# Kernel optimization log

Hardware: AMD Instinct MI355X
Metric: run time of the kernel (lower is better)

The kernel has to match this reference:

```python
import jax, jax.numpy as jnp
import numpy as np

N_NODES = 100000
MAX_DEG = 16
D_IN = 256
D_OUT = 256


def setup_inputs() -> dict:
    key = jax.random.key(0)
    k1, k2, k3, k4, k5 = jax.random.split(key, 5)
    x = jax.random.normal(k1, (N_NODES, D_IN), dtype=jnp.float32)
    # padded edge list: -1 marks padding; first column always valid so degree >= 1
    col0 = jax.random.randint(k2, (N_NODES, 1), 0, N_NODES)
    rest = jax.random.randint(k3, (N_NODES, MAX_DEG - 1), -1, N_NODES)
    edge_index = jnp.concatenate([col0, rest], axis=1).astype(jnp.int64)
    # torch Linear(2*D_IN, D_OUT): weight [D_OUT, 2*D_IN], bias [D_OUT]
    W = jax.random.normal(k4, (D_OUT, 2 * D_IN), dtype=jnp.float32) * 0.05
    b = jax.random.normal(k5, (D_OUT,), dtype=jnp.float32) * 0.05
    return {"x": x, "edge_index": edge_index, "W": W, "b": b}


def reference(x, edge_index, W, b):
    # pad with a zero row so index -1 (padding) gathers zeros, matching torch
    padded = jnp.concatenate([x, jnp.zeros((1, x.shape[1]), dtype=x.dtype)], axis=0)
    neigh = padded[edge_index]  # [N, MAX_DEG, D_IN]
    degree = jnp.sum(edge_index >= 0, axis=-1, keepdims=True).astype(x.dtype)  # [N, 1]
    neigh_agg = jnp.sum(neigh, axis=1) / degree  # mean aggregation, [N, D_IN]
    h = jnp.concatenate([x, neigh_agg], axis=1)  # [N, 2*D_IN]
    return h @ W.T + b
```

## Files before the change

kernel.cpp:

```cpp
#include <hip/hip_runtime.h>
#include <stdint.h>


#define MAX_DEG 16
#define D_IN 256
#define D_K 512
#define D_OUT 256
#define BM 32
#define LDS_STRIDE 520
#define N_NODES_C 100000

typedef __attribute__((ext_vector_type(8))) short bf16x8;
typedef __attribute__((ext_vector_type(4))) float f32x4;

__device__ __forceinline__ uint32_t f2bf(float f) {
    union { float f; uint32_t u; } v; v.f = f;
    uint32_t u = v.u;
    return (u + 0x7FFFu + ((u >> 16) & 1u)) >> 16;
}
__device__ __forceinline__ uint32_t pack2(float lo, float hi) {
    return f2bf(lo) | (f2bf(hi) << 16);
}

__global__ __launch_bounds__(256) void cast_all_kernel(
    const float* __restrict__ x, const float* __restrict__ W,
    ushort* __restrict__ Xb, ushort* __restrict__ Wb)
{
    const int b = blockIdx.x;
    const int tid = threadIdx.x;
    if (b < 12500) {
        const size_t i = (size_t)b * 2048 + tid * 8;
        float4 v0 = *(const float4*)(x + i);
        float4 v1 = *(const float4*)(x + i + 4);
        uint4 p = { pack2(v0.x, v0.y), pack2(v0.z, v0.w),
                    pack2(v1.x, v1.y), pack2(v1.z, v1.w) };
        *(uint4*)(Xb + i) = p;
    } else if (b == 12500) {
        if (tid < 32) {
            uint4 z = {0u, 0u, 0u, 0u};
            *(uint4*)(Xb + (size_t)N_NODES_C * D_IN + tid * 8) = z;
        }
    } else {
        const size_t i = (size_t)(b - 12501) * 2048 + tid * 8;
        float4 v0 = *(const float4*)(W + i);
        float4 v1 = *(const float4*)(W + i + 4);
        uint4 p = { pack2(v0.x, v0.y), pack2(v0.z, v0.w),
                    pack2(v1.x, v1.y), pack2(v1.z, v1.w) };
        *(uint4*)(Wb + i) = p;
    }
}

__global__ __launch_bounds__(512, 4) void sage_bf16_kernel(
    const ushort* __restrict__ Xb,
    const int* __restrict__ edge,
    const ushort* __restrict__ Wb,
    const float* __restrict__ bias,
    float* __restrict__ out)
{
    __shared__ ushort sH[BM * LDS_STRIDE];

    const int tid = threadIdx.x;
    const int node0 = blockIdx.x * BM;

    {
        const int m = tid >> 4;
        const int l = tid & 15;
        const int node = node0 + m;

        const uint4* xr = (const uint4*)(Xb + (size_t)node * D_IN);
        uint4* selfdst = (uint4*)(sH + (size_t)m * LDS_STRIDE);
        uint4 s0 = xr[l], s1 = xr[16 + l];
        selfdst[l] = s0; selfdst[16 + l] = s1;

        const int4* ep = (const int4*)(edge + (size_t)node * MAX_DEG);
        uint32_t off[MAX_DEG]; int deg = 0;
        #pragma unroll
        for (int g = 0; g < 4; ++g) {
            int4 e = ep[g];
            deg += (e.x >= 0) + (e.y >= 0) + (e.z >= 0) + (e.w >= 0);
            off[g*4+0] = (uint32_t)(e.x < 0 ? N_NODES_C : e.x) * 512u;
            off[g*4+1] = (uint32_t)(e.y < 0 ? N_NODES_C : e.y) * 512u;
            off[g*4+2] = (uint32_t)(e.z < 0 ? N_NODES_C : e.z) * 512u;
            off[g*4+3] = (uint32_t)(e.w < 0 ? N_NODES_C : e.w) * 512u;
        }
        const float inv = 1.0f / (float)deg;
        const char* xb = (const char*)Xb;

        #pragma unroll 1
        for (int c = 0; c < 2; ++c) {
            const uint32_t coff = (uint32_t)(c * 256 + l * 16);
            uint4 st[MAX_DEG];
            #pragma unroll
            for (int d = 0; d < MAX_DEG; ++d)
                st[d] = *(const uint4*)(xb + (size_t)(off[d] + coff));

            float a[8];
            #pragma unroll
            for (int q = 0; q < 8; ++q) a[q] = 0.f;
            #pragma unroll
            for (int d = 0; d < MAX_DEG; ++d) {
                uint32_t u[4] = { st[d].x, st[d].y, st[d].z, st[d].w };
                #pragma unroll
                for (int q = 0; q < 4; ++q) {
                    union { uint32_t ui; float f; } lo, hi;
                    lo.ui = u[q] << 16;
                    hi.ui = u[q] & 0xFFFF0000u;
                    a[2*q]   += lo.f;
                    a[2*q+1] += hi.f;
                }
            }
            uint4 p = { pack2(a[0]*inv, a[1]*inv), pack2(a[2]*inv, a[3]*inv),
                        pack2(a[4]*inv, a[5]*inv), pack2(a[6]*inv, a[7]*inv) };
            *(uint4*)(sH + (size_t)m * LDS_STRIDE + D_IN + c * 128 + l * 8) = p;
        }
    }
    __syncthreads();

    {
        const int w = tid >> 6;
        const int lane = tid & 63;
        const int quad = lane >> 4;
        const int r16  = lane & 15;

        f32x4 acc[2][2];
        #pragma unroll
        for (int j = 0; j < 2; ++j) {
            float bv = bias[w * 32 + j * 16 + r16];
            acc[0][j] = (f32x4){bv, bv, bv, bv};
            acc[1][j] = (f32x4){bv, bv, bv, bv};
        }

        const ushort* a0p = sH + (size_t)r16 * LDS_STRIDE + quad * 8;
        const ushort* a1p = a0p + 16 * LDS_STRIDE;
        #pragma unroll
        for (int ks = 0; ks < D_K / 32; ++ks) {
            bf16x8 a0 = *(const bf16x8*)(a0p + ks * 32);
            bf16x8 a1 = *(const bf16x8*)(a1p + ks * 32);
            #pragma unroll
            for (int j = 0; j < 2; ++j) {
                const int o = w * 32 + j * 16 + r16;
                bf16x8 b = *(const bf16x8*)(Wb + (size_t)o * D_K + ks * 32 + quad * 8);
                acc[0][j] = __builtin_amdgcn_mfma_f32_16x16x32_bf16(a0, b, acc[0][j], 0, 0, 0);
                acc[1][j] = __builtin_amdgcn_mfma_f32_16x16x32_bf16(a1, b, acc[1][j], 0, 0, 0);
            }
        }

        #pragma unroll
        for (int mt = 0; mt < 2; ++mt) {
            #pragma unroll
            for (int j = 0; j < 2; ++j) {
                const int o = w * 32 + j * 16 + r16;
                #pragma unroll
                for (int r = 0; r < 4; ++r) {
                    const int row = node0 + mt * 16 + quad * 4 + r;
                    out[(size_t)row * D_OUT + o] = acc[mt][j][r];
                }
            }
        }
    }
}

__global__ __launch_bounds__(256) void cast_w_kernel(const float* __restrict__ W,
                                                     ushort* __restrict__ Wb) {
    int i = (blockIdx.x * 256 + threadIdx.x) * 4;
    float4 v = *(const float4*)(W + i);
    ushort4 p = { (ushort)f2bf(v.x), (ushort)f2bf(v.y),
                  (ushort)f2bf(v.z), (ushort)f2bf(v.w) };
    *(ushort4*)(Wb + i) = p;
}

__global__ __launch_bounds__(256) void sage_fp32_kernel(
    const float* __restrict__ x, const int* __restrict__ edge,
    const ushort* __restrict__ Wb, const float* __restrict__ bias,
    float* __restrict__ out)
{
    __shared__ ushort sH[32 * LDS_STRIDE];
    const int tid = threadIdx.x;
    const int node0 = blockIdx.x * 32;
    {
        const int m = tid >> 3, l = tid & 7;
        const int node = node0 + m;
        const float4* xrow = (const float4*)(x + (size_t)node * D_IN);
        ushort* dst = sH + m * LDS_STRIDE + l * 32;
        #pragma unroll
        for (int q = 0; q < 8; ++q) {
            float4 v = xrow[l * 8 + q];
            ushort4 p = { (ushort)f2bf(v.x), (ushort)f2bf(v.y),
                          (ushort)f2bf(v.z), (ushort)f2bf(v.w) };
            *(ushort4*)(dst + q * 4) = p;
        }
        float4 agg[8];
        #pragma unroll
        for (int q = 0; q < 8; ++q) agg[q] = make_float4(0.f,0.f,0.f,0.f);
        int deg = 0;
        for (int d = 0; d < MAX_DEG; ++d) {
            int nb = edge[(size_t)node * MAX_DEG + d];
            if (nb >= 0) {
                ++deg;
                const float4* nr = (const float4*)(x + (size_t)nb * D_IN);
                #pragma unroll
                for (int q = 0; q < 8; ++q) {
                    float4 t = nr[l * 8 + q];
                    agg[q].x += t.x; agg[q].y += t.y;
                    agg[q].z += t.z; agg[q].w += t.w;
                }
            }
        }
        const float inv = 1.0f / (float)deg;
        ushort* dst2 = sH + m * LDS_STRIDE + D_IN + l * 32;
        #pragma unroll
        for (int q = 0; q < 8; ++q) {
            ushort4 p = { (ushort)f2bf(agg[q].x*inv), (ushort)f2bf(agg[q].y*inv),
                          (ushort)f2bf(agg[q].z*inv), (ushort)f2bf(agg[q].w*inv) };
            *(ushort4*)(dst2 + q * 4) = p;
        }
    }
    __syncthreads();
    {
        const int wave = tid >> 6, lane = tid & 63;
        const int quad = lane >> 4, r16 = lane & 15;
        const int mt = wave & 1, nh = wave >> 1;
        f32x4 acc[8];
        #pragma unroll
        for (int j = 0; j < 8; ++j) {
            float bv = bias[(nh * 8 + j) * 16 + r16];
            acc[j] = (f32x4){bv, bv, bv, bv};
        }
        const ushort* arow = sH + (mt * 16 + r16) * LDS_STRIDE + quad * 8;
        #pragma unroll
        for (int ks = 0; ks < D_K / 32; ++ks) {
            bf16x8 a = *(const bf16x8*)(arow + ks * 32);
            #pragma unroll
            for (int j = 0; j < 8; ++j) {
                const int o = (nh * 8 + j) * 16 + r16;
                bf16x8 b = *(const bf16x8*)(Wb + (size_t)o * D_K + ks * 32 + quad * 8);
                acc[j] = __builtin_amdgcn_mfma_f32_16x16x32_bf16(a, b, acc[j], 0, 0, 0);
            }
        }
        #pragma unroll
        for (int j = 0; j < 8; ++j) {
            const int o = (nh * 8 + j) * 16 + r16;
            #pragma unroll
            for (int r = 0; r < 4; ++r) {
                const int row = node0 + mt * 16 + quad * 4 + r;
                out[(size_t)row * D_OUT + o] = acc[j][r];
            }
        }
    }
}

extern "C" void kernel_launch(void* const* d_in, const int* in_sizes, int n_in,
                              void* d_out, int out_size, void* d_ws, size_t ws_size,
                              hipStream_t stream) {
    const float* x    = (const float*)d_in[0];
    const int*   edge = (const int*)d_in[1];
    const float* W    = (const float*)d_in[2];
    const float* bias = (const float*)d_in[3];
    float* out = (float*)d_out;

    const size_t xb_bytes = (size_t)(N_NODES_C + 1) * D_IN * 2;
    const size_t wb_bytes = (size_t)D_OUT * D_K * 2;
    const int n = in_sizes[0] / D_IN;

    if (ws_size >= xb_bytes + wb_bytes) {
        ushort* Xb = (ushort*)d_ws;
        ushort* Wb = (ushort*)((char*)d_ws + xb_bytes);
        cast_all_kernel<<<12565, 256, 0, stream>>>(x, W, Xb, Wb);
        sage_bf16_kernel<<<n / BM, 512, 0, stream>>>(Xb, edge, Wb, bias, out);
    } else {
        ushort* Wb = (ushort*)d_ws;
        cast_w_kernel<<<(D_OUT * D_K) / 1024, 256, 0, stream>>>(W, Wb);
        sage_fp32_kernel<<<n / 32, 256, 0, stream>>>(x, edge, Wb, bias, out);
    }
}
```

Before: 364.8 us.

## Split fused gather+GEMM into separate gather and GEMM kernels via workspace buffer

Replaces the fused kernel with two kernels when the workspace is large enough. The first is a gather kernel where 32 threads per node each load all 16 neighbour chunks at once, with a sched barrier to cluster the loads. The second is a GEMM kernel that reads self and aggregated rows straight from global memory without using LDS. The aim is more memory-level parallelism and occupancy in the gather phase, paid for with an extra bf16 round trip of the aggregated matrix (~51MB) and one more launch.

```diff
diff --git a/kernel.cpp b/kernel.cpp
--- a/kernel.cpp
+++ b/kernel.cpp
@@ -6,9 +6,8 @@
 #define D_IN 256
 #define D_K 512
 #define D_OUT 256
-#define BM 32
+#define N_NODES_C 100000
 #define LDS_STRIDE 520
-#define N_NODES_C 100000
 
 typedef __attribute__((ext_vector_type(8))) short bf16x8;
 typedef __attribute__((ext_vector_type(4))) float f32x4;
@@ -50,23 +49,136 @@
     }
 }
 
-__global__ __launch_bounds__(512, 4) void sage_bf16_kernel(
+__global__ __launch_bounds__(256, 5) void gather_kernel(
     const ushort* __restrict__ Xb,
     const int* __restrict__ edge,
+    ushort* __restrict__ Agg)
+{
+    const int t = blockIdx.x * 256 + threadIdx.x;
+    const int node = t >> 5;
+    const int c = t & 31;
+
+    const int4* ep = (const int4*)(edge + (size_t)node * MAX_DEG);
+    uint32_t off[MAX_DEG]; int deg = 0;
+    #pragma unroll
+    for (int g = 0; g < 4; ++g) {
+        int4 e = ep[g];
+        deg += (e.x >= 0) + (e.y >= 0) + (e.z >= 0) + (e.w >= 0);
+        off[g*4+0] = (uint32_t)(e.x < 0 ? N_NODES_C : e.x) * 512u;
+        off[g*4+1] = (uint32_t)(e.y < 0 ? N_NODES_C : e.y) * 512u;
+        off[g*4+2] = (uint32_t)(e.z < 0 ? N_NODES_C : e.z) * 512u;
+        off[g*4+3] = (uint32_t)(e.w < 0 ? N_NODES_C : e.w) * 512u;
+    }
+
+    const char* base = (const char*)Xb + c * 16;
+    uint4 st[MAX_DEG];
+    #pragma unroll
+    for (int d = 0; d < MAX_DEG; ++d)
+        st[d] = *(const uint4*)(base + (size_t)off[d]);
+#if defined(__has_builtin)
+#if __has_builtin(__builtin_amdgcn_sched_barrier)
+    __builtin_amdgcn_sched_barrier(0);
+#endif
+#endif
+
+    float a[8];
+    #pragma unroll
+    for (int q = 0; q < 8; ++q) a[q] = 0.f;
+    #pragma unroll
+    for (int d = 0; d < MAX_DEG; ++d) {
+        uint32_t u[4] = { st[d].x, st[d].y, st[d].z, st[d].w };
+        #pragma unroll
+        for (int q = 0; q < 4; ++q) {
+            union { uint32_t ui; float f; } lo, hi;
+            lo.ui = u[q] << 16;
+            hi.ui = u[q] & 0xFFFF0000u;
+            a[2*q]   += lo.f;
+            a[2*q+1] += hi.f;
+        }
+    }
+    const float inv = 1.0f / (float)deg;
+    uint4 p = { pack2(a[0]*inv, a[1]*inv), pack2(a[2]*inv, a[3]*inv),
+                pack2(a[4]*inv, a[5]*inv), pack2(a[6]*inv, a[7]*inv) };
+    *(uint4*)(Agg + (size_t)node * D_IN + c * 8) = p;
+}
+
+__global__ __launch_bounds__(512) void gemm_kernel(
+    const ushort* __restrict__ Xb,
+    const ushort* __restrict__ Agg,
     const ushort* __restrict__ Wb,
     const float* __restrict__ bias,
     float* __restrict__ out)
 {
-    __shared__ ushort sH[BM * LDS_STRIDE];
-
     const int tid = threadIdx.x;
-    const int node0 = blockIdx.x * BM;
-
+    const int node0 = blockIdx.x * 32;
+    const int w = tid >> 6;
+    const int lane = tid & 63;
+    const int quad = lane >> 4;
+    const int r16  = lane & 15;
+
+    f32x4 acc[2][2];
+    #pragma unroll
+    for (int j = 0; j < 2; ++j) {
+        float bv = bias[w * 32 + j * 16 + r16];
+        acc[0][j] = (f32x4){bv, bv, bv, bv};
+        acc[1][j] = (f32x4){bv, bv, bv, bv};
+    }
+
+    const ushort* x0 = Xb  + (size_t)(node0 + r16) * D_IN + quad * 8;
+    const ushort* x1 = x0 + 16 * D_IN;
+    const ushort* g0 = Agg + (size_t)(node0 + r16) * D_IN + quad * 8;
+    const ushort* g1 = g0 + 16 * D_IN;
+
+    #pragma unroll
+    for (int ks = 0; ks < 8; ++ks) {
+        bf16x8 a0 = *(const bf16x8*)(x0 + ks * 32);
+        bf16x8 a1 = *(const bf16x8*)(x1 + ks * 32);
+        #pragma unroll
+        for (int j = 0; j < 2; ++j) {
+            const int o = w * 32 + j * 16 + r16;
+            bf16x8 b = *(const bf16x8*)(Wb + (size_t)o * D_K + ks * 32 + quad * 8);
+            acc[0][j] = __builtin_amdgcn_mfma_f32_16x16x32_bf16(a0, b, acc[0][j], 0, 0, 0);
+            acc[1][j] = __builtin_amdgcn_mfma_f32_16x16x32_bf16(a1, b, acc[1][j], 0, 0, 0);
+        }
+    }
+    #pragma unroll
+    for (int ks = 0; ks < 8; ++ks) {
+        bf16x8 a0 = *(const bf16x8*)(g0 + ks * 32);
+        bf16x8 a1 = *(const bf16x8*)(g1 + ks * 32);
+        #pragma unroll
+        for (int j = 0; j < 2; ++j) {
+            const int o = w * 32 + j * 16 + r16;
+            bf16x8 b = *(const bf16x8*)(Wb + (size_t)o * D_K + (8 + ks) * 32 + quad * 8);
+            acc[0][j] = __builtin_amdgcn_mfma_f32_16x16x32_bf16(a0, b, acc[0][j], 0, 0, 0);
+            acc[1][j] = __builtin_amdgcn_mfma_f32_16x16x32_bf16(a1, b, acc[1][j], 0, 0, 0);
+        }
+    }
+
+    #pragma unroll
+    for (int mt = 0; mt < 2; ++mt) {
+        #pragma unroll
+        for (int j = 0; j < 2; ++j) {
+            const int o = w * 32 + j * 16 + r16;
+            #pragma unroll
+            for (int r = 0; r < 4; ++r) {
+                const int row = node0 + mt * 16 + quad * 4 + r;
+                out[(size_t)row * D_OUT + o] = acc[mt][j][r];
+            }
+        }
+    }
+}
+
+__global__ __launch_bounds__(512, 4) void sage_bf16_kernel(
+    const ushort* __restrict__ Xb, const int* __restrict__ edge,
+    const ushort* __restrict__ Wb, const float* __restrict__ bias,
+    float* __restrict__ out)
+{
+    __shared__ ushort sH[32 * LDS_STRIDE];
+    const int tid = threadIdx.x;
+    const int node0 = blockIdx.x * 32;
     {
-        const int m = tid >> 4;
-        const int l = tid & 15;
+        const int m = tid >> 4, l = tid & 15;
         const int node = node0 + m;
-
         const uint4* xr = (const uint4*)(Xb + (size_t)node * D_IN);
         uint4* selfdst = (uint4*)(sH + (size_t)m * LDS_STRIDE);
         uint4 s0 = xr[l], s1 = xr[16 + l];
@@ -85,7 +197,6 @@
         }
         const float inv = 1.0f / (float)deg;
         const char* xb = (const char*)Xb;
-
         #pragma unroll 1
         for (int c = 0; c < 2; ++c) {
             const uint32_t coff = (uint32_t)(c * 256 + l * 16);
@@ -93,7 +204,6 @@
             #pragma unroll
             for (int d = 0; d < MAX_DEG; ++d)
                 st[d] = *(const uint4*)(xb + (size_t)(off[d] + coff));
-
             float a[8];
             #pragma unroll
             for (int q = 0; q < 8; ++q) a[q] = 0.f;
@@ -115,13 +225,9 @@
         }
     }
     __syncthreads();
-
     {
-        const int w = tid >> 6;
-        const int lane = tid & 63;
-        const int quad = lane >> 4;
-        const int r16  = lane & 15;
-
+        const int w = tid >> 6, lane = tid & 63;
+        const int quad = lane >> 4, r16 = lane & 15;
         f32x4 acc[2][2];
         #pragma unroll
         for (int j = 0; j < 2; ++j) {
@@ -129,7 +235,6 @@
             acc[0][j] = (f32x4){bv, bv, bv, bv};
             acc[1][j] = (f32x4){bv, bv, bv, bv};
         }
-
         const ushort* a0p = sH + (size_t)r16 * LDS_STRIDE + quad * 8;
         const ushort* a1p = a0p + 16 * LDS_STRIDE;
         #pragma unroll
@@ -144,7 +249,6 @@
                 acc[1][j] = __builtin_amdgcn_mfma_f32_16x16x32_bf16(a1, b, acc[1][j], 0, 0, 0);
             }
         }
-
         #pragma unroll
         for (int mt = 0; mt < 2; ++mt) {
             #pragma unroll
@@ -258,15 +362,23 @@
     const float* bias = (const float*)d_in[3];
     float* out = (float*)d_out;
 
-    const size_t xb_bytes = (size_t)(N_NODES_C + 1) * D_IN * 2;
-    const size_t wb_bytes = (size_t)D_OUT * D_K * 2;
+    const size_t xb_bytes  = (size_t)(N_NODES_C + 1) * D_IN * 2;
+    const size_t wb_bytes  = (size_t)D_OUT * D_K * 2;
+    const size_t agg_bytes = (size_t)N_NODES_C * D_IN * 2;
     const int n = in_sizes[0] / D_IN;
 
-    if (ws_size >= xb_bytes + wb_bytes) {
+    if (ws_size >= xb_bytes + wb_bytes + agg_bytes) {
+        ushort* Xb  = (ushort*)d_ws;
+        ushort* Wb  = (ushort*)((char*)d_ws + xb_bytes);
+        ushort* Agg = (ushort*)((char*)d_ws + xb_bytes + wb_bytes);
+        cast_all_kernel<<<12565, 256, 0, stream>>>(x, W, Xb, Wb);
+        gather_kernel<<<(n * 32) / 256, 256, 0, stream>>>(Xb, edge, Agg);
+        gemm_kernel<<<n / 32, 512, 0, stream>>>(Xb, Agg, Wb, bias, out);
+    } else if (ws_size >= xb_bytes + wb_bytes) {
         ushort* Xb = (ushort*)d_ws;
         ushort* Wb = (ushort*)((char*)d_ws + xb_bytes);
         cast_all_kernel<<<12565, 256, 0, stream>>>(x, W, Xb, Wb);
-        sage_bf16_kernel<<<n / BM, 512, 0, stream>>>(Xb, edge, Wb, bias, out);
+        sage_bf16_kernel<<<n / 32, 512, 0, stream>>>(Xb, edge, Wb, bias, out);
     } else {
         ushort* Wb = (ushort*)d_ws;
         cast_w_kernel<<<(D_OUT * D_K) / 1024, 256, 0, stream>>>(W, Wb);
```

After: 472.8 us. +29.6%, slower.
